# Optimization experiments

Measured on AMD Instinct MI355X. Metric: run time of the kernel, lower is better.

## Reference

```python
import jax, jax.numpy as jnp
import numpy as np

IN_F, H1, H2, NC = 784, 1024, 1024, 10
BATCH = 32
EPS = 0.1


def setup_inputs() -> dict:
    key = jax.random.key(0)
    ks = jax.random.split(key, 8)
    x = jax.random.normal(ks[0], (BATCH, IN_F), jnp.float32)
    y = jax.random.randint(ks[1], (BATCH,), 0, NC)
    W1 = jax.random.normal(ks[2], (H1, IN_F), jnp.float32) / np.float32(np.sqrt(IN_F))
    b1 = jax.random.normal(ks[3], (H1,), jnp.float32) * 0.01
    W2 = jax.random.normal(ks[4], (H2, H1), jnp.float32) / np.float32(np.sqrt(H1))
    b2 = jax.random.normal(ks[5], (H2,), jnp.float32) * 0.01
    W3 = jax.random.normal(ks[6], (NC, H2), jnp.float32) / np.float32(np.sqrt(H2))
    b3 = jax.random.normal(ks[7], (NC,), jnp.float32) * 0.01
    return dict(x=x, y=y, W1=W1, b1=b1, W2=W2, b2=b2, W3=W3, b3=b3)


def _relu_coeffs(zl, zu):
    # d = 1 where zl>=0, zu/(zu-zl) where crossing, 0 where zu<=0 (as in select_layer)
    I = (zl < 0) & (zu > 0)
    d = jnp.where(zl >= 0, 1.0, jnp.where(I, zu / (zu - zl), 0.0))
    lI = jnp.where(I, zl, 0.0)  # zl restricted to crossing set I
    return d, lI


def reference(x, y, W1, b1, W2, b2, W3, b3):
    eps = jnp.float32(EPS)
    # ---- layer-1 preactivation bounds (InfBall fval) ----
    nom1 = x @ W1.T + b1                              # [B,H1]
    r1 = eps * jnp.abs(W1).sum(1)                     # [H1]
    zl1, zu1 = nom1 - r1, nom1 + r1
    d1, l1m = _relu_coeffs(zl1, zu1)                  # [B,H1]

    # ---- layer-2 preactivation bounds via dual (transpose) propagation, nu = I ----
    nu1 = W2[None, :, :] * d1[:, None, :]             # [B,H2,H1]  (D1 W2^T rows)
    V0 = jnp.einsum('bji,ik->bjk', nu1, W1)           # [B,H2,IN]
    A = jnp.einsum('bjk,bk->bj', V0, x) + b2 + nu1 @ b1
    E = eps * jnp.abs(V0).sum(-1)
    crossl = jnp.einsum('bji,bi->bj', jax.nn.relu(-nu1), l1m)
    crossu = jnp.einsum('bji,bi->bj', jax.nn.relu(nu1), l1m)
    zl2 = A - E + crossl
    zu2 = A + E - crossu
    d2, l2m = _relu_coeffs(zl2, zu2)                  # [B,H2]

    # ---- final robust bounds: c[b,j,:] = e_{y_b} - e_j ----
    eye = jnp.eye(NC, dtype=x.dtype)
    c = eye[y][:, None, :] - eye[None, :, :]          # [B,NC,NC]
    nu2 = (c @ W3) * d2[:, None, :]                   # [B,NC,H2]
    nu1f = (nu2 @ W2) * d1[:, None, :]                # [B,NC,H1]
    V0f = nu1f @ W1                                   # [B,NC,IN]
    Af = jnp.einsum('bjk,bk->bj', V0f, x) + c @ b3 + nu2 @ b2 + nu1f @ b1
    Ef = eps * jnp.abs(V0f).sum(-1)
    crossf = (jnp.einsum('bji,bi->bj', jax.nn.relu(-nu2), l2m)
              + jnp.einsum('bji,bi->bj', jax.nn.relu(-nu1f), l1m))
    J = Af - Ef + crossf                              # lower bound of c^T z
    return -J                                         # f: upper bound of z_j - z_y, [B,NC]
```

## Files before the change

### kernel.cpp

```cpp
#include <hip/hip_runtime.h>
#include <math.h>

#define B    32
#define INF  784
#define H1   1024
#define H2   1024
#define NC   10
#define EPSV 0.1f

typedef __attribute__((ext_vector_type(8))) short short8;
typedef __attribute__((ext_vector_type(4))) float floatx4;

__device__ inline ushort bf16_rne(float f) {
  uint u = __builtin_bit_cast(uint, f);
  u += 0x7FFFu + ((u >> 16) & 1u);
  return (ushort)(u >> 16);
}
__device__ inline uint pack2(float a, float b) {
  return (uint)bf16_rne(a) | ((uint)bf16_rne(b) << 16);
}
__device__ inline uint scale_pack(uint u, float d0, float d1v) {
  float f0 = __builtin_bit_cast(float, u << 16) * d0;
  float f1 = __builtin_bit_cast(float, u & 0xFFFF0000u) * d1v;
  uint r0 = __builtin_bit_cast(uint, f0) + 0x8000u;
  uint r1 = __builtin_bit_cast(uint, f1) + 0x8000u;
  return __builtin_amdgcn_perm(r1, r0, 0x07060302u);
}

__global__ __launch_bounds__(256) void k_pre(
    const float* __restrict__ x, const float* __restrict__ W1,
    const float* __restrict__ b1, const float* __restrict__ W2,
    ushort* __restrict__ W1F, ushort* __restrict__ W2F,
    float* __restrict__ d1B, float* __restrict__ t1B, float* __restrict__ dnB,
    float* __restrict__ Ezero)
{
  __shared__ float red[4][B + 1];
  __shared__ float Ts[4][32][17];
  int bid = blockIdx.x;
  int t = threadIdx.x;
  if (bid < 64) {
    int jt = bid;
    int lane = t & 63, c0 = t >> 6;
    int l15 = lane & 15, quad = lane >> 4;
    for (int c = c0; c < 32; c += 4) {
      const float* src = &W2[(size_t)(jt * 16 + l15) * H1 + c * 32 + quad * 8];
      float4 v0 = *reinterpret_cast<const float4*>(src);
      float4 v1 = *reinterpret_cast<const float4*>(src + 4);
      uint4 o;
      o.x = pack2(v0.x, v0.y); o.y = pack2(v0.z, v0.w);
      o.z = pack2(v1.x, v1.y); o.w = pack2(v1.z, v1.w);
      *reinterpret_cast<uint4*>(&W2F[((size_t)(c * 64 + jt) * 64 + lane) * 8]) = o;
    }
  } else if (bid < 113) {
    int mt = bid - 64;
    int col0 = mt * 16;
    int w = t >> 6, lane = t & 63;
    int l15 = lane & 15, quad = lane >> 4;
    for (int cg = 0; cg < 8; cg++) {
      int c = cg * 4 + w;
#pragma unroll
      for (int p = 0; p < 8; p++) {
        int r = p * 4 + (lane >> 4);
        Ts[w][r][lane & 15] = W1[(size_t)(c * 32 + r) * INF + col0 + (lane & 15)];
      }
      float f[8];
#pragma unroll
      for (int e = 0; e < 8; e++) f[e] = Ts[w][quad * 8 + e][l15];
      uint4 o;
      o.x = pack2(f[0], f[1]); o.y = pack2(f[2], f[3]);
      o.z = pack2(f[4], f[5]); o.w = pack2(f[6], f[7]);
      *reinterpret_cast<uint4*>(&W1F[((size_t)(c * 49 + mt) * 64 + lane) * 8]) = o;
    }
  } else if (bid < 1137) {
    int i = bid - 113;
    const float* w = W1 + (size_t)i * INF;
    float acc[B];
#pragma unroll
    for (int b = 0; b < B; b++) acc[b] = 0.f;
    float wabs = 0.f;
    for (int k = t; k < INF; k += 256) {
      float wv = w[k];
      wabs += fabsf(wv);
#pragma unroll
      for (int b = 0; b < B; b++) acc[b] = fmaf(x[b * INF + k], wv, acc[b]);
    }
#pragma unroll
    for (int off = 32; off > 0; off >>= 1) {
#pragma unroll
      for (int b = 0; b < B; b++) acc[b] += __shfl_down(acc[b], off, 64);
      wabs += __shfl_down(wabs, off, 64);
    }
    int wave = t >> 6, lane = t & 63;
    if (lane == 0) {
#pragma unroll
      for (int b = 0; b < B; b++) red[wave][b] = acc[b];
      red[wave][B] = wabs;
    }
    __syncthreads();
    if (t < B) {
      float s = red[0][t] + red[1][t] + red[2][t] + red[3][t];
      float r = EPSV * (red[0][B] + red[1][B] + red[2][B] + red[3][B]);
      float nom = s + b1[i];
      float zl = nom - r, zu = nom + r;
      float d, l;
      if (zl >= 0.f)      { d = 1.f;            l = 0.f; }
      else if (zu > 0.f)  { d = zu / (zu - zl); l = zl;  }
      else                { d = 0.f;            l = 0.f; }
      d1B[(size_t)t * H1 + i] = d;
      t1B[(size_t)t * H1 + i] = d * l;
      dnB[(size_t)t * H1 + i] = d * nom;
    }
  } else {
    int zb = bid - 1137;
    for (int idx = t; idx < 8192; idx += 256) {
      int pos = zb * 8192 + idx;
      if (pos < 54272) Ezero[pos] = 0.f;
    }
  }
}

#define K3_LOAD(c, A, Bv) do {                                                  \
  _Pragma("unroll")                                                             \
  for (int ni = 0; ni < 2; ni++)                                                \
    Bv[ni] = *reinterpret_cast<const uint4*>(bBase + (size_t)(c) * 32768 + ni * 512); \
  _Pragma("unroll")                                                             \
  for (int mi = 0; mi < 7; mi++)                                                \
    A[mi] = *reinterpret_cast<const uint4*>(aBase + (size_t)(c) * 25088 + mi * 512); \
} while (0)

#define K3F_COMP(c, A, Bv, DsRow, accB) do {                                    \
  float4 dv0 = *reinterpret_cast<const float4*>(&DsRow[(c) * 32]);              \
  float4 dv1 = *reinterpret_cast<const float4*>(&DsRow[(c) * 32 + 4]);          \
  short8 bfr[2];                                                                \
  _Pragma("unroll")                                                             \
  for (int ni = 0; ni < 2; ni++) {                                              \
    uint4 sb;                                                                   \
    sb.x = scale_pack(Bv[ni].x, dv0.x, dv0.y);                                  \
    sb.y = scale_pack(Bv[ni].y, dv0.z, dv0.w);                                  \
    sb.z = scale_pack(Bv[ni].z, dv1.x, dv1.y);                                  \
    sb.w = scale_pack(Bv[ni].w, dv1.z, dv1.w);                                  \
    bfr[ni] = __builtin_bit_cast(short8, sb);                                   \
  }                                                                             \
  _Pragma("unroll")                                                             \
  for (int mi = 0; mi < 7; mi++) {                                              \
    short8 af = __builtin_bit_cast(short8, A[mi]);                              \
    _Pragma("unroll")                                                           \
    for (int ni = 0; ni < 2; ni++)                                              \
      accB[mi][ni] = __builtin_amdgcn_mfma_f32_16x16x32_bf16(af, bfr[ni], accB[mi][ni], 0, 0, 0); \
  }                                                                             \
} while (0)

__global__ __launch_bounds__(256, 2) void k3(
    const ushort* __restrict__ W1F, const ushort* __restrict__ W2F,
    const float* __restrict__ d1B, float* __restrict__ E)
{
  int b0 = blockIdx.z * 2;
  int t = threadIdx.x, w = t >> 6, lane = t & 63;
  int quad = lane >> 4, l15 = lane & 15;
  int mt0 = blockIdx.x * 7;
  int jt0 = blockIdx.y * 8 + w * 2;

  __shared__ float Ds[2][H1];
  for (int idx = t; idx < 2 * H1; idx += 256)
    Ds[idx >> 10][idx & 1023] = d1B[(size_t)(b0 + (idx >> 10)) * H1 + (idx & 1023)];
  __syncthreads();

  const ushort* aBase = W1F + ((size_t)mt0 * 64 + lane) * 8;
  const ushort* bBase = W2F + ((size_t)jt0 * 64 + lane) * 8;
  const float* Ds0 = &Ds[0][quad * 8];
  const float* Ds1 = &Ds[1][quad * 8];

  floatx4 acc[2][7][2];
#pragma unroll
  for (int bb = 0; bb < 2; bb++)
#pragma unroll
    for (int mi = 0; mi < 7; mi++)
#pragma unroll
      for (int ni = 0; ni < 2; ni++) acc[bb][mi][ni] = (floatx4){0.f, 0.f, 0.f, 0.f};

  uint4 a0[7], b0v[2], a1[7], b1v[2];
  K3_LOAD(0, a0, b0v);
  K3_LOAD(1, a1, b1v);
  for (int c = 0; c < 30; c += 2) {
    K3F_COMP(c, a0, b0v, Ds0, acc[0]);
    K3F_COMP(c, a0, b0v, Ds1, acc[1]);
    K3_LOAD(c + 2, a0, b0v);
    K3F_COMP(c + 1, a1, b1v, Ds0, acc[0]);
    K3F_COMP(c + 1, a1, b1v, Ds1, acc[1]);
    if (c + 3 < 32) K3_LOAD(c + 3, a1, b1v);
  }
  K3F_COMP(30, a0, b0v, Ds0, acc[0]);
  K3F_COMP(30, a0, b0v, Ds1, acc[1]);
  K3F_COMP(31, a1, b1v, Ds0, acc[0]);
  K3F_COMP(31, a1, b1v, Ds1, acc[1]);

#pragma unroll
  for (int bb = 0; bb < 2; bb++) {
#pragma unroll
    for (int ni = 0; ni < 2; ni++) {
      float s = 0.f;
#pragma unroll
      for (int mi = 0; mi < 7; mi++)
#pragma unroll
        for (int r = 0; r < 4; r++) s += fabsf(acc[bb][mi][ni][r]);
      s += __shfl_xor(s, 16, 64);
      s += __shfl_xor(s, 32, 64);
      if (lane < 16) {
        int j = (jt0 + ni) * 16 + l15;
        atomicAdd(&E[(size_t)j * B + b0 + bb], EPSV * s);
      }
    }
  }
}

__global__ __launch_bounds__(256) void k245a(
    const float* __restrict__ W2, const float* __restrict__ b2,
    const float* __restrict__ dnB, const float* __restrict__ t1B,
    const float* __restrict__ E, const float* __restrict__ W3,
    const int* __restrict__ y,
    float* __restrict__ nu2T, float* __restrict__ F2)
{
  int j = blockIdx.x;
  int t = threadIdx.x;
  int wave = t >> 6, lane = t & 63;
  int b0 = wave * 8;
  float aA[8] = {}, aCl[8] = {}, aCu[8] = {};
  const float* __restrict__ w2 = W2 + (size_t)j * H1;
  for (int i = lane; i < H1; i += 64) {
    float wv = w2[i];
    float wp = fmaxf(wv, 0.f), wn = fmaxf(-wv, 0.f);
#pragma unroll
    for (int r = 0; r < 8; r++) {
      float dv = dnB[(size_t)(b0 + r) * H1 + i];
      float tv = t1B[(size_t)(b0 + r) * H1 + i];
      aA[r]  = fmaf(wv, dv, aA[r]);
      aCl[r] = fmaf(wn, tv, aCl[r]);
      aCu[r] = fmaf(wp, tv, aCu[r]);
    }
  }
#pragma unroll
  for (int off = 32; off > 0; off >>= 1) {
#pragma unroll
    for (int r = 0; r < 8; r++) {
      aA[r]  += __shfl_down(aA[r],  off, 64);
      aCl[r] += __shfl_down(aCl[r], off, 64);
      aCu[r] += __shfl_down(aCu[r], off, 64);
    }
  }
  __shared__ float sA[B], sCl[B], sCu[B];
  __shared__ float sd2[B], st2[B], sdb[B], swy[B], sw3[NC];
  float bj = b2[j];
  if (lane == 0) {
#pragma unroll
    for (int r = 0; r < 8; r++) {
      sA [b0 + r] = aA[r] + bj;
      sCl[b0 + r] = aCl[r];
      sCu[b0 + r] = aCu[r];
    }
  }
  if (t >= 64 && t < 96)   swy[t - 64]  = W3[(size_t)y[t - 64] * H2 + j];
  if (t >= 128 && t < 138) sw3[t - 128] = W3[(size_t)(t - 128) * H2 + j];
  __syncthreads();
  if (t < B) {
    float a = sA[t], e = E[(size_t)j * B + t];
    float zl = a - e + sCl[t];
    float zu = a + e - sCu[t];
    float d, l;
    if (zl >= 0.f)      { d = 1.f;            l = 0.f; }
    else if (zu > 0.f)  { d = zu / (zu - zl); l = zl;  }
    else                { d = 0.f;            l = 0.f; }
    sd2[t] = d;
    st2[t] = d * l;
    sdb[t] = d * bj;
  }
  __syncthreads();
  for (int tt = t; tt < B * NC; tt += 256) {
    int b = tt / NC, jc = tt - b * NC;
    float cw = swy[b] - sw3[jc];
    float d2v = sd2[b];
    nu2T[((size_t)b * H2 + j) * 12 + jc] = cw * d2v;
    float val = cw * sdb[b] + fmaxf(-cw, 0.f) * st2[b];
    atomicAdd(&F2[((size_t)(j & 63) * B + b) * NC + jc], val);
  }
}

__global__ __launch_bounds__(256) void k5b1(
    const float* __restrict__ W2, const float* __restrict__ nu2T,
    float* __restrict__ hpart)
{
  int t = threadIdx.x;
  int i1 = blockIdx.x * 512 + t * 2;
  int b = blockIdx.y, s = blockIdx.z;
  const float* __restrict__ nrowb = nu2T + ((size_t)b * H2 + s * 128) * 12;
  const float* __restrict__ w2b = W2 + (size_t)s * 128 * H1 + i1;
  float h0[NC] = {}, h1[NC] = {};
  for (int i2 = 0; i2 < 128; i2++) {
    float2 wv = *reinterpret_cast<const float2*>(&w2b[(size_t)i2 * H1]);
    const float* __restrict__ nrow = nrowb + i2 * 12;
#pragma unroll
    for (int j = 0; j < NC; j++) {
      h0[j] = fmaf(nrow[j], wv.x, h0[j]);
      h1[j] = fmaf(nrow[j], wv.y, h1[j]);
    }
  }
#pragma unroll
  for (int j = 0; j < NC; j++) {
    float2 o; o.x = h0[j]; o.y = h1[j];
    *reinterpret_cast<float2*>(&hpart[(((size_t)s * B + b) * NC + j) * H1 + i1]) = o;
  }
}

__global__ __launch_bounds__(256) void k5b2(
    const float* __restrict__ hpart,
    const float* __restrict__ d1B, const float* __restrict__ t1B,
    const float* __restrict__ dnB,
    float* __restrict__ nu1fT, float* __restrict__ F)
{
  int t = threadIdx.x;
  int i1 = blockIdx.x * 256 + t;
  int b = blockIdx.y;
  float d1v = d1B[(size_t)b * H1 + i1];
  float t1v = t1B[(size_t)b * H1 + i1];
  float dnv = dnB[(size_t)b * H1 + i1];
  float sn[NC], c1[NC];
#pragma unroll
  for (int j = 0; j < NC; j++) {
    float hv = 0.f;
#pragma unroll
    for (int s = 0; s < 8; s++)
      hv += hpart[(((size_t)s * B + b) * NC + j) * H1 + i1];
    nu1fT[((size_t)b * H1 + i1) * 12 + j] = hv * d1v;
    sn[j] = hv * dnv;
    c1[j] = fmaxf(-hv, 0.f) * t1v;
  }
#pragma unroll
  for (int off = 32; off > 0; off >>= 1) {
#pragma unroll
    for (int j = 0; j < NC; j++) {
      sn[j] += __shfl_down(sn[j], off, 64);
      c1[j] += __shfl_down(c1[j], off, 64);
    }
  }
  __shared__ float red[4][2 * NC];
  int wave = t >> 6, lane = t & 63;
  if (lane == 0) {
#pragma unroll
    for (int j = 0; j < NC; j++) { red[wave][j] = sn[j]; red[wave][NC + j] = c1[j]; }
  }
  __syncthreads();
  if (t < NC) {
    float s = 0.f;
    for (int w = 0; w < 4; w++) s += red[w][t] + red[w][NC + t];
    atomicAdd(&F[b * NC + t], s);
  }
}

__global__ __launch_bounds__(128) void k5c1(
    const float* __restrict__ W1, const float* __restrict__ nu1fT,
    float* __restrict__ ppart)
{
  int t = threadIdx.x;
  bool valid = (t < 112);
  int k = blockIdx.x * 112 + (valid ? t : 0);
  int b = blockIdx.y, s = blockIdx.z;
  const float* __restrict__ nrowb = nu1fT + ((size_t)b * H1 + s * 128) * 12;
  const float* __restrict__ w1b = W1 + (size_t)s * 128 * INF + k;
  float acc[NC] = {};
  for (int i1 = 0; i1 < 128; i1++) {
    float w1v = w1b[(size_t)i1 * INF];
    const float* __restrict__ nrow = nrowb + i1 * 12;
#pragma unroll
    for (int j = 0; j < NC; j++) acc[j] = fmaf(nrow[j], w1v, acc[j]);
  }
  if (valid) {
#pragma unroll
    for (int j = 0; j < NC; j++)
      ppart[(((size_t)s * B + b) * NC + j) * INF + k] = acc[j];
  }
}

__global__ __launch_bounds__(256) void k5c2_out(
    const float* __restrict__ ppart, const float* __restrict__ F,
    const float* __restrict__ F2, const float* __restrict__ b3,
    const int* __restrict__ y, float* __restrict__ out)
{
  int b = blockIdx.x;
  int t = threadIdx.x;
  float e[NC] = {};
  for (int k = t; k < INF; k += 256) {
#pragma unroll
    for (int j = 0; j < NC; j++) {
      float v = 0.f;
#pragma unroll
      for (int s = 0; s < 8; s++)
        v += ppart[(((size_t)s * B + b) * NC + j) * INF + k];
      e[j] += fabsf(v);
    }
  }
#pragma unroll
  for (int off = 32; off > 0; off >>= 1) {
#pragma unroll
    for (int j = 0; j < NC; j++) e[j] += __shfl_down(e[j], off, 64);
  }
  __shared__ float red[4][NC];
  int wave = t >> 6, lane = t & 63;
  if (lane == 0) {
#pragma unroll
    for (int j = 0; j < NC; j++) red[wave][j] = e[j];
  }
  __syncthreads();
  if (t < NC) {
    float ef = 0.f;
    for (int w = 0; w < 4; w++) ef += red[w][t];
    float s = F[b * NC + t];
    for (int slot = 0; slot < 64; slot++)
      s += F2[((size_t)slot * B + b) * NC + t];
    int yb = y[b];
    s += b3[yb] - b3[t];
    out[b * NC + t] = EPSV * ef - s;
  }
}

extern "C" void kernel_launch(void* const* d_in, const int* in_sizes, int n_in,
                              void* d_out, int out_size, void* d_ws, size_t ws_size,
                              hipStream_t stream) {
  const float* x  = (const float*)d_in[0];
  const int*   y  = (const int*)  d_in[1];
  const float* W1 = (const float*)d_in[2];
  const float* b1 = (const float*)d_in[3];
  const float* W2 = (const float*)d_in[4];
  const float* b2 = (const float*)d_in[5];
  const float* W3 = (const float*)d_in[6];
  const float* b3 = (const float*)d_in[7];
  float* out = (float*)d_out;
  float* ws  = (float*)d_ws;

  float* d1B  = ws;
  float* t1B  = ws + 32768;
  float* dnB  = ws + 65536;
  float* E    = ws + 196608;
  float* F    = ws + 229376;
  float* F2   = ws + 230400;
  float* nu2T = ws + 328704;
  ushort* W2F = (ushort*)(ws + 721920);
  ushort* W1F = (ushort*)(ws + 1246208);
  float* nu1fT = ws + 328704;
  float* hpart = ws + 721920;
  float* ppart = ws + 721920;

  k_pre<<<1144, 256, 0, stream>>>(x, W1, b1, W2, W1F, W2F, d1B, t1B, dnB, E);
  k3<<<dim3(7, 8, 16), 256, 0, stream>>>(W1F, W2F, d1B, E);
  k245a<<<H2, 256, 0, stream>>>(W2, b2, dnB, t1B, E, W3, y, nu2T, F2);
  k5b1<<<dim3(2, B, 8), 256, 0, stream>>>(W2, nu2T, hpart);
  k5b2<<<dim3(4, B), 256, 0, stream>>>(hpart, d1B, t1B, dnB, nu1fT, F);
  k5c1<<<dim3(7, B, 8), 128, 0, stream>>>(W1, nu1fT, ppart);
  k5c2_out<<<B, 256, 0, stream>>>(ppart, F, F2, b3, y, out);
}
```

Before: 213.2 us.

## Pre-scale W2 per batch into workspace and run two-batch plain MFMA GEMM

```diff
diff --git a/kernel.cpp b/kernel.cpp
--- a/kernel.cpp
+++ b/kernel.cpp
@@ -119,6 +119,117 @@
   }
 }
 
+__global__ __launch_bounds__(256) void k3s(
+    const ushort* __restrict__ W2F, const float* __restrict__ d1B,
+    ushort* __restrict__ W2D)
+{
+  int bid = blockIdx.x;
+  int xcd = bid & 7, q = bid >> 3;
+  int c = xcd * 4 + (q >> 5);
+  int b = q & 31;
+  int t = threadIdx.x, w = t >> 6, lane = t & 63;
+  int quad = lane >> 4;
+  __shared__ float ds[32];
+  if (t < 32) ds[t] = d1B[(size_t)b * H1 + c * 32 + t];
+  __syncthreads();
+  float4 dv0 = *reinterpret_cast<const float4*>(&ds[quad * 8]);
+  float4 dv1 = *reinterpret_cast<const float4*>(&ds[quad * 8 + 4]);
+  const ushort* src = W2F + ((size_t)(c * 64) * 64 + lane) * 8;
+  ushort* dst = W2D + (size_t)b * 1048576 + ((size_t)(c * 64) * 64 + lane) * 8;
+  for (int jt = w; jt < 64; jt += 4) {
+    uint4 u = *reinterpret_cast<const uint4*>(src + (size_t)jt * 512);
+    uint4 o;
+    o.x = scale_pack(u.x, dv0.x, dv0.y);
+    o.y = scale_pack(u.y, dv0.z, dv0.w);
+    o.z = scale_pack(u.z, dv1.x, dv1.y);
+    o.w = scale_pack(u.w, dv1.z, dv1.w);
+    *reinterpret_cast<uint4*>(dst + (size_t)jt * 512) = o;
+  }
+}
+
+#define K3D_LOAD(c, A, B0, B1) do {                                             \
+  _Pragma("unroll")                                                             \
+  for (int ni = 0; ni < 2; ni++) {                                              \
+    B0[ni] = *reinterpret_cast<const uint4*>(bBase0 + (size_t)(c) * 32768 + ni * 512); \
+    B1[ni] = *reinterpret_cast<const uint4*>(bBase1 + (size_t)(c) * 32768 + ni * 512); \
+  }                                                                             \
+  _Pragma("unroll")                                                             \
+  for (int mi = 0; mi < 7; mi++)                                                \
+    A[mi] = *reinterpret_cast<const uint4*>(aBase + (size_t)(c) * 25088 + mi * 512); \
+} while (0)
+
+#define K3D_COMP(A, Bv, accB) do {                                              \
+  _Pragma("unroll")                                                             \
+  for (int mi = 0; mi < 7; mi++) {                                              \
+    short8 af = __builtin_bit_cast(short8, A[mi]);                              \
+    _Pragma("unroll")                                                           \
+    for (int ni = 0; ni < 2; ni++)                                              \
+      accB[mi][ni] = __builtin_amdgcn_mfma_f32_16x16x32_bf16(af, __builtin_bit_cast(short8, Bv[ni]), accB[mi][ni], 0, 0, 0); \
+  }                                                                             \
+} while (0)
+
+__global__ __launch_bounds__(256, 2) void k3d(
+    const ushort* __restrict__ W1F, const ushort* __restrict__ W2D,
+    float* __restrict__ E)
+{
+  int bid = blockIdx.x;
+  int xcd = bid & 7, q = bid >> 3;
+  int x = q % 7;
+  int yz = xcd * 16 + q / 7;
+  int by = yz & 7, bz = yz >> 3;
+  int b0 = bz * 2;
+  int t = threadIdx.x, w = t >> 6, lane = t & 63;
+  int l15 = lane & 15;
+  int mt0 = x * 7;
+  int jt0 = by * 8 + w * 2;
+
+  const ushort* aBase = W1F + ((size_t)mt0 * 64 + lane) * 8;
+  const ushort* bBase0 = W2D + (size_t)b0 * 1048576 + ((size_t)jt0 * 64 + lane) * 8;
+  const ushort* bBase1 = bBase0 + 1048576;
+
+  floatx4 acc[2][7][2];
+#pragma unroll
+  for (int bb = 0; bb < 2; bb++)
+#pragma unroll
+    for (int mi = 0; mi < 7; mi++)
+#pragma unroll
+      for (int ni = 0; ni < 2; ni++) acc[bb][mi][ni] = (floatx4){0.f, 0.f, 0.f, 0.f};
+
+  uint4 a0[7], a1[7], p00[2], p01[2], p10[2], p11[2];
+  K3D_LOAD(0, a0, p00, p01);
+  K3D_LOAD(1, a1, p10, p11);
+  for (int c = 0; c < 30; c += 2) {
+    K3D_COMP(a0, p00, acc[0]);
+    K3D_COMP(a0, p01, acc[1]);
+    K3D_LOAD(c + 2, a0, p00, p01);
+    K3D_COMP(a1, p10, acc[0]);
+    K3D_COMP(a1, p11, acc[1]);
+    if (c + 3 < 32) K3D_LOAD(c + 3, a1, p10, p11);
+  }
+  K3D_COMP(a0, p00, acc[0]);
+  K3D_COMP(a0, p01, acc[1]);
+  K3D_COMP(a1, p10, acc[0]);
+  K3D_COMP(a1, p11, acc[1]);
+
+#pragma unroll
+  for (int bb = 0; bb < 2; bb++) {
+#pragma unroll
+    for (int ni = 0; ni < 2; ni++) {
+      float s = 0.f;
+#pragma unroll
+      for (int mi = 0; mi < 7; mi++)
+#pragma unroll
+        for (int r = 0; r < 4; r++) s += fabsf(acc[bb][mi][ni][r]);
+      s += __shfl_xor(s, 16, 64);
+      s += __shfl_xor(s, 32, 64);
+      if (lane < 16) {
+        int j = (jt0 + ni) * 16 + l15;
+        atomicAdd(&E[(size_t)j * B + b0 + bb], EPSV * s);
+      }
+    }
+  }
+}
+
 #define K3_LOAD(c, A, Bv) do {                                                  \
   _Pragma("unroll")                                                             \
   for (int ni = 0; ni < 2; ni++)                                                \
@@ -447,9 +558,17 @@
   float* nu1fT = ws + 328704;
   float* hpart = ws + 721920;
   float* ppart = ws + 721920;
+  const size_t W2D_OFF = 1648640;
+  ushort* W2D = (ushort*)(ws + W2D_OFF);
+  const size_t WS_NEED = (W2D_OFF + 16777216) * sizeof(float);
 
   k_pre<<<1144, 256, 0, stream>>>(x, W1, b1, W2, W1F, W2F, d1B, t1B, dnB, E);
-  k3<<<dim3(7, 8, 16), 256, 0, stream>>>(W1F, W2F, d1B, E);
+  if (ws_size >= WS_NEED) {
+    k3s<<<1024, 256, 0, stream>>>(W2F, d1B, W2D);
+    k3d<<<896, 256, 0, stream>>>(W1F, W2D, E);
+  } else {
+    k3<<<dim3(7, 8, 16), 256, 0, stream>>>(W1F, W2F, d1B, E);
+  }
   k245a<<<H2, 256, 0, stream>>>(W2, b2, dnB, t1B, E, W3, y, nu2T, F2);
   k5b1<<<dim3(2, B, 8), 256, 0, stream>>>(W2, nu2T, hpart);
   k5b2<<<dim3(4, B), 256, 0, stream>>>(hpart, d1B, t1B, dnB, nu1fT, F);
```

After: 223.0 us. +4.6%, slower.
